# Performance work log

Measured on AMD Instinct MI355X. Metric: run time of the kernel, lower is better.

The kernel has to match this reference:

```python
import jax, jax.numpy as jnp
import numpy as np

B, C, W, H = 4, 64, 64, 64
CH = 64  # ch == input_nc so residual is valid

def setup_inputs() -> dict:
    key = jax.random.key(0)
    ks = jax.random.split(key, 5)
    return {
        "x": jax.random.normal(ks[0], (B, C, W, H), jnp.float32),
        "y": jax.random.normal(ks[1], (B, C, W, H), jnp.float32),
        "Wf": jax.random.normal(ks[2], (CH // 2, C), jnp.float32) * 0.05,
        "bf": jnp.zeros((CH // 2,), jnp.float32),
        "Wg": jax.random.normal(ks[3], (CH // 2, C), jnp.float32) * 0.05,
        "bg": jnp.zeros((CH // 2,), jnp.float32),
        "Wh": jax.random.normal(ks[4], (CH, C), jnp.float32) * 0.05,
        "bh": jnp.zeros((CH,), jnp.float32),
        "gamma": jnp.full((1,), 0.5, jnp.float32),
    }

def reference(x, y, Wf, bf, Wg, bg, Wh, bh, gamma):
    b, c, w, h = x.shape
    n = w * h
    xf = x.reshape(b, c, n)   # [b, C, N]
    yf = y.reshape(b, c, n)
    # 1x1 convs == per-pixel linear maps over channels
    f = jnp.einsum('oc,bcn->bon', Wf, xf) + bf[None, :, None]   # [b, CH/2, N]
    g = jnp.einsum('oc,bcn->bon', Wg, yf) + bg[None, :, None]   # [b, CH/2, N]
    hv = jnp.einsum('oc,bcn->bon', Wh, yf) + bh[None, :, None]  # [b, CH,   N]
    # s = g^T @ f : [b, N, N]
    s = jnp.einsum('bcm,bcn->bmn', g, f)
    beta = jax.nn.softmax(s, axis=-1)
    # o = beta @ h^T : [b, N, CH]
    o = jnp.einsum('bmn,bcn->bmc', beta, hv)
    o = o.transpose(0, 2, 1).reshape(b, -1, w, h)  # [b, CH, w, h]
    return gamma[0] * o + x
```

## Files before the change

### kernel.cpp

```cpp
#include <hip/hip_runtime.h>
#include <hip/hip_bf16.h>

#define BB  4
#define CC  64
#define NN  4096
#define CF  32
#define CHN 64

typedef __attribute__((ext_vector_type(8)))  __bf16 bf16x8;
typedef __attribute__((ext_vector_type(4)))  __bf16 bf16x4;
typedef __attribute__((ext_vector_type(4)))  float  floatx4;
typedef __attribute__((ext_vector_type(16))) float  floatx16;
typedef __attribute__((ext_vector_type(2)))  unsigned int uintx2;
typedef __attribute__((ext_vector_type(4)))  unsigned int uintx4;

__device__ __forceinline__ float scrub(float v) {
    return fminf(fmaxf(v, -1e30f), 1e30f);
}

__device__ __forceinline__ unsigned cvt_pk_bf16(float lo, float hi) {
    unsigned r;
    asm("v_cvt_pk_bf16_f32 %0, %1, %2" : "=v"(r) : "v"(lo), "v"(hi));
    return r;
}

__global__ __launch_bounds__(256) void prep_kernel(
    const float* __restrict__ x, const float* __restrict__ y,
    const float* __restrict__ Wf, const float* __restrict__ bfp,
    const float* __restrict__ Wg, const float* __restrict__ bgp,
    const float* __restrict__ Wh, const float* __restrict__ bhp,
    __bf16* __restrict__ fT, __bf16* __restrict__ gT, __bf16* __restrict__ hvb)
{
    __shared__ __align__(16) __bf16 wbf[128][72];
    __shared__ float sbias[128];

    const int t  = threadIdx.x;
    const int w  = t >> 6;
    const int l  = t & 63;
    const int lo = l & 15;
    const int q  = l >> 4;

    const int b   = blockIdx.x >> 7;
    const int nb  = blockIdx.x & 127;
    const int nn  = nb * 32 + (w & 1) * 16 + lo;
    const int ctbase = (w < 2) ? 0 : 4;

    for (int i = t; i < 128 * CC; i += 256) {
        int row = i >> 6, c = i & 63;
        float wv;
        if (row < 32)      wv = Wf[(size_t)row * CC + c];
        else if (row < 64) wv = Wg[(size_t)(row - 32) * CC + c];
        else               wv = Wh[(size_t)(row - 64) * CC + c];
        wbf[row][c] = (__bf16)wv;
    }
    if (t < 128) {
        if (t < 32)      sbias[t] = bfp[t];
        else if (t < 64) sbias[t] = bgp[t - 32];
        else             sbias[t] = bhp[t - 64];
    }
    __syncthreads();

    const float* xb = x + (size_t)b * CC * NN;
    const float* yb = y + (size_t)b * CC * NN;
    bf16x8 bx[2], by[2];
    #pragma unroll
    for (int kh = 0; kh < 2; kh++) {
        #pragma unroll
        for (int j = 0; j < 8; j++) {
            int c = kh * 32 + q * 8 + j;
            by[kh][j] = (__bf16)yb[(size_t)c * NN + nn];
        }
    }
    if (w < 2) {
        #pragma unroll
        for (int kh = 0; kh < 2; kh++)
            #pragma unroll
            for (int j = 0; j < 8; j++) {
                int c = kh * 32 + q * 8 + j;
                bx[kh][j] = (__bf16)xb[(size_t)c * NN + nn];
            }
    }

    const floatx4 zero4 = {0.f, 0.f, 0.f, 0.f};
    #pragma unroll
    for (int cti = 0; cti < 4; cti++) {
        const int ct = ctbase + cti;
        const bf16x8* src = (ct < 2) ? bx : by;
        floatx4 acc = zero4;
        #pragma unroll
        for (int kh = 0; kh < 2; kh++) {
            const bf16x8 a = *(const bf16x8*)&wbf[ct*16 + lo][kh*32 + q*8];
            acc = __builtin_amdgcn_mfma_f32_16x16x32_bf16(a, src[kh], acc, 0, 0, 0);
        }
        if (ct < 4) {
            bf16x4 pk;
            #pragma unroll
            for (int r = 0; r < 4; r++)
                pk[r] = (__bf16)(acc[r] + sbias[ct*16 + q*4 + r]);
            __bf16* dstbase = (ct < 2) ? fT : gT;
            int cho = (ct & 1) * 16;
            *(bf16x4*)&dstbase[((size_t)b * NN + nn) * CF + cho + q*4] = pk;
        } else {
            #pragma unroll
            for (int r = 0; r < 4; r++) {
                int ch = (ct - 4) * 16 + q*4 + r;
                hvb[((size_t)b * CHN + ch) * NN + nn] =
                    (__bf16)(acc[r] + sbias[64 + ch]);
            }
        }
    }
}

__global__ __launch_bounds__(512, 2) void attn_kernel(
    const __bf16* __restrict__ fT, const __bf16* __restrict__ gT,
    const __bf16* __restrict__ hvb,
    const float* __restrict__ x, const float* __restrict__ gamma_p,
    float* __restrict__ out)
{
    __shared__ float osum[8][64][67];
    __shared__ float lsum[512];

    const int t   = threadIdx.x;
    const int w   = t >> 6;
    const int l   = t & 63;
    const int l31 = l & 31;
    const int hi  = l >> 5;

    const int slot = blockIdx.x;
    const int xcd  = slot & 7;
    const int b    = xcd >> 1;
    const int mg   = ((xcd & 1) << 5) | (slot >> 3);
    const int m0   = mg * 64;

    const __bf16* fb = fT  + (size_t)b * NN * CF;
    const __bf16* gb = gT  + (size_t)b * NN * CF;
    const __bf16* hb = hvb + (size_t)b * CHN * NN;

    bf16x8 bg_[2][2];
    #pragma unroll
    for (int mt = 0; mt < 2; mt++)
        #pragma unroll
        for (int kk = 0; kk < 2; kk++)
            bg_[mt][kk] = *(const bf16x8*)(gb + (size_t)(m0 + mt*32 + l31) * CF + kk*16 + hi*8);

    const floatx16 zero16 = {};
    floatx16 oacc[2][2];
    #pragma unroll
    for (int mt = 0; mt < 2; mt++)
        #pragma unroll
        for (int ct = 0; ct < 2; ct++) oacc[mt][ct] = zero16;
    float rsum[2] = {0.f, 0.f};

    for (int i = 0; i < 8; i++) {
        const int n0 = (8*i + w) * 64;

        bf16x8 af[2][2];
        #pragma unroll
        for (int nt = 0; nt < 2; nt++)
            #pragma unroll
            for (int kk = 0; kk < 2; kk++)
                af[nt][kk] = *(const bf16x8*)(fb + (size_t)(n0 + nt*32 + l31) * CF + kk*16 + hi*8);

        bf16x8 bv[2][4];
        #pragma unroll
        for (int ct = 0; ct < 2; ct++)
            #pragma unroll
            for (int ks = 0; ks < 4; ks++)
                bv[ct][ks] = *(const bf16x8*)(hb + (size_t)(ct*32 + l31) * NN + n0 + ks*16 + hi*8);

        bf16x8 pa[2][4];
        #pragma unroll
        for (int mt = 0; mt < 2; mt++) {
            #pragma unroll
            for (int nt = 0; nt < 2; nt++) {
                floatx16 s = __builtin_amdgcn_mfma_f32_32x32x16_bf16(
                    af[nt][0], bg_[mt][0], zero16, 0, 0, 0);
                s = __builtin_amdgcn_mfma_f32_32x32x16_bf16(
                    af[nt][1], bg_[mt][1], s, 0, 0, 0);

                float p[16];
                #pragma unroll
                for (int r = 0; r < 16; r++) p[r] = __expf(s[r]);

                unsigned W[8];
                #pragma unroll
                for (int g = 0; g < 8; g++) W[g] = cvt_pk_bf16(p[2*g], p[2*g+1]);

                #pragma unroll
                for (int g = 0; g < 8; g++)
                    rsum[mt] += __uint_as_float(W[g] << 16)
                              + __uint_as_float(W[g] & 0xffff0000u);

                uintx2 s02 = __builtin_amdgcn_permlane32_swap(W[0], W[2], false, false);
                uintx2 s13 = __builtin_amdgcn_permlane32_swap(W[1], W[3], false, false);
                uintx2 s46 = __builtin_amdgcn_permlane32_swap(W[4], W[6], false, false);
                uintx2 s57 = __builtin_amdgcn_permlane32_swap(W[5], W[7], false, false);

                uintx4 w0 = {s02.x, s13.x, s02.y, s13.y};
                uintx4 w1 = {s46.x, s57.x, s46.y, s57.y};
                pa[mt][nt*2 + 0] = __builtin_bit_cast(bf16x8, w0);
                pa[mt][nt*2 + 1] = __builtin_bit_cast(bf16x8, w1);
            }
        }

        #pragma unroll
        for (int mt = 0; mt < 2; mt++)
            #pragma unroll
            for (int ct = 0; ct < 2; ct++)
                #pragma unroll
                for (int ks = 0; ks < 4; ks++)
                    oacc[mt][ct] = __builtin_amdgcn_mfma_f32_32x32x16_bf16(
                        pa[mt][ks], bv[ct][ks], oacc[mt][ct], 0, 0, 0);
    }

    #pragma unroll
    for (int mt = 0; mt < 2; mt++)
        rsum[mt] += __shfl_xor(rsum[mt], 32, 64);

    #pragma unroll
    for (int mt = 0; mt < 2; mt++) {
        #pragma unroll
        for (int ct = 0; ct < 2; ct++)
            #pragma unroll
            for (int r = 0; r < 16; r++)
                osum[w][mt*32 + ((r&3) + 8*(r>>2) + 4*hi)][ct*32 + l31] =
                    oacc[mt][ct][r];
        if (hi == 0)
            lsum[w*64 + mt*32 + l31] = rsum[mt];
    }
    __syncthreads();

    const float gam = gamma_p[0];
    const int m  = t & 63;
    const int cb = t >> 6;
    float lt = 0.f;
    #pragma unroll
    for (int s = 0; s < 8; s++) lt += lsum[s*64 + m];
    const float inv = 1.f / lt;
    #pragma unroll
    for (int it = 0; it < 8; it++) {
        const int ch = it*8 + cb;
        float acc = 0.f;
        #pragma unroll
        for (int s = 0; s < 8; s++) acc += osum[s][m][ch];
        size_t gi = ((size_t)b * CHN + ch) * NN + m0 + m;
        float ov = scrub(acc * inv);
        out[gi] = gam * ov + x[gi];
    }
}

extern "C" void kernel_launch(void* const* d_in, const int* in_sizes, int n_in,
                              void* d_out, int out_size, void* d_ws, size_t ws_size,
                              hipStream_t stream)
{
    const float* x     = (const float*)d_in[0];
    const float* y     = (const float*)d_in[1];
    const float* Wf    = (const float*)d_in[2];
    const float* bf    = (const float*)d_in[3];
    const float* Wg    = (const float*)d_in[4];
    const float* bg    = (const float*)d_in[5];
    const float* Wh    = (const float*)d_in[6];
    const float* bh    = (const float*)d_in[7];
    const float* gamma = (const float*)d_in[8];
    float* out = (float*)d_out;

    __bf16* wsb = (__bf16*)d_ws;
    __bf16* fT  = wsb;
    __bf16* gT  = fT + (size_t)BB * NN * CF;
    __bf16* hvb = gT + (size_t)BB * NN * CF;

    prep_kernel<<<dim3(BB * 128), dim3(256), 0, stream>>>(
        x, y, Wf, bf, Wg, bg, Wh, bh, fT, gT, hvb);
    attn_kernel<<<dim3(BB * 64), dim3(512), 0, stream>>>(
        fT, gT, hvb, x, gamma, out);
}
```

Baseline: 100.5 us.

## Fuse projection and attention kernels with a software grid barrier

Merges the prep and attention kernels into one persistent kernel of 256 blocks. A global atomic-counter grid barrier separates the 1x1-conv projection phase from the attention phase, and shared memory is reused between the two phases. Folds log2(e) into g so the softmax can use the raw v_exp_f32 instruction. The row sum now accumulates the fp32 exponentials instead of the bf16-rounded ones. This removes a kernel launch and the gap between kernels. The risk is a deadlock if all 256 blocks are not co-resident, plus the cost of barrier spinning.

```diff
diff --git a/kernel.cpp b/kernel.cpp
--- a/kernel.cpp
+++ b/kernel.cpp
@@ -6,6 +6,8 @@
 #define NN  4096
 #define CF  32
 #define CHN 64
+
+#define LOG2E 1.4426950408889634f
 
 typedef __attribute__((ext_vector_type(8)))  __bf16 bf16x8;
 typedef __attribute__((ext_vector_type(4)))  __bf16 bf16x4;
@@ -23,114 +25,136 @@
     asm("v_cvt_pk_bf16_f32 %0, %1, %2" : "=v"(r) : "v"(lo), "v"(hi));
     return r;
 }
-
-__global__ __launch_bounds__(256) void prep_kernel(
+__device__ __forceinline__ float exp2_f32(float x) {
+    float r;
+    asm("v_exp_f32 %0, %1" : "=v"(r) : "v"(x));
+    return r;
+}
+
+__device__ unsigned g_cnt = 0;
+__device__ unsigned g_gen = 0;
+
+__device__ __forceinline__ void grid_barrier() {
+    __syncthreads();
+    if (threadIdx.x == 0) {
+        __threadfence();
+        unsigned my = atomicAdd(&g_cnt, 1u);
+        unsigned target = (my >> 8) + 1;
+        if ((my & 255u) == 255u) {
+            __hip_atomic_store(&g_gen, target, __ATOMIC_RELEASE,
+                               __HIP_MEMORY_SCOPE_AGENT);
+        } else {
+            while ((int)(__hip_atomic_load(&g_gen, __ATOMIC_ACQUIRE,
+                                           __HIP_MEMORY_SCOPE_AGENT) - target) < 0)
+                __builtin_amdgcn_s_sleep(1);
+        }
+        __threadfence();
+    }
+    __syncthreads();
+}
+
+__global__ __launch_bounds__(512, 2) void fused_kernel(
     const float* __restrict__ x, const float* __restrict__ y,
     const float* __restrict__ Wf, const float* __restrict__ bfp,
     const float* __restrict__ Wg, const float* __restrict__ bgp,
     const float* __restrict__ Wh, const float* __restrict__ bhp,
-    __bf16* __restrict__ fT, __bf16* __restrict__ gT, __bf16* __restrict__ hvb)
+    __bf16* __restrict__ fT, __bf16* __restrict__ gT, __bf16* __restrict__ hvb,
+    const float* __restrict__ gamma_p, float* __restrict__ out)
 {
-    __shared__ __align__(16) __bf16 wbf[128][72];
-    __shared__ float sbias[128];
-
-    const int t  = threadIdx.x;
-    const int w  = t >> 6;
-    const int l  = t & 63;
-    const int lo = l & 15;
-    const int q  = l >> 4;
-
-    const int b   = blockIdx.x >> 7;
-    const int nb  = blockIdx.x & 127;
-    const int nn  = nb * 32 + (w & 1) * 16 + lo;
-    const int ctbase = (w < 2) ? 0 : 4;
-
-    for (int i = t; i < 128 * CC; i += 256) {
-        int row = i >> 6, c = i & 63;
-        float wv;
-        if (row < 32)      wv = Wf[(size_t)row * CC + c];
-        else if (row < 64) wv = Wg[(size_t)(row - 32) * CC + c];
-        else               wv = Wh[(size_t)(row - 64) * CC + c];
-        wbf[row][c] = (__bf16)wv;
-    }
-    if (t < 128) {
-        if (t < 32)      sbias[t] = bfp[t];
-        else if (t < 64) sbias[t] = bgp[t - 32];
-        else             sbias[t] = bhp[t - 64];
-    }
-    __syncthreads();
-
-    const float* xb = x + (size_t)b * CC * NN;
-    const float* yb = y + (size_t)b * CC * NN;
-    bf16x8 bx[2], by[2];
-    #pragma unroll
-    for (int kh = 0; kh < 2; kh++) {
-        #pragma unroll
-        for (int j = 0; j < 8; j++) {
-            int c = kh * 32 + q * 8 + j;
-            by[kh][j] = (__bf16)yb[(size_t)c * NN + nn];
-        }
-    }
-    if (w < 2) {
+    __shared__ __align__(16) char smem[8*64*67*4 + 512*4];
+    __bf16 (*wbf)[72]      = (__bf16 (*)[72])smem;
+    float*  sbias          = (float*)(smem + 128*72*2);
+    float (*osum)[64][67]  = (float (*)[64][67])smem;
+    float*  lsum           = (float*)(smem + 8*64*67*4);
+
+    const int t = threadIdx.x;
+
+    const int slot = blockIdx.x;
+    const int xcd  = slot & 7;
+    const int b    = xcd >> 1;
+    const int mg   = ((xcd & 1) << 5) | (slot >> 3);
+
+    {
+        const int w  = t >> 6;
+        const int l  = t & 63;
+        const int lo = l & 15;
+        const int q  = l >> 4;
+        const int nn = mg * 64 + (w & 3) * 16 + lo;
+        const int ctbase = (w >> 2) * 4;
+
+        for (int i = t; i < 128 * CC; i += 512) {
+            int row = i >> 6, c = i & 63;
+            float wv;
+            if (row < 32)      wv = Wf[(size_t)row * CC + c];
+            else if (row < 64) wv = Wg[(size_t)(row - 32) * CC + c];
+            else               wv = Wh[(size_t)(row - 64) * CC + c];
+            wbf[row][c] = (__bf16)wv;
+        }
+        if (t < 128) {
+            if (t < 32)      sbias[t] = bfp[t];
+            else if (t < 64) sbias[t] = bgp[t - 32];
+            else             sbias[t] = bhp[t - 64];
+        }
+        __syncthreads();
+
+        const float* xb = x + (size_t)b * CC * NN;
+        const float* yb = y + (size_t)b * CC * NN;
+        bf16x8 bx[2], by[2];
         #pragma unroll
         for (int kh = 0; kh < 2; kh++)
             #pragma unroll
             for (int j = 0; j < 8; j++) {
                 int c = kh * 32 + q * 8 + j;
-                bx[kh][j] = (__bf16)xb[(size_t)c * NN + nn];
-            }
-    }
-
-    const floatx4 zero4 = {0.f, 0.f, 0.f, 0.f};
-    #pragma unroll
-    for (int cti = 0; cti < 4; cti++) {
-        const int ct = ctbase + cti;
-        const bf16x8* src = (ct < 2) ? bx : by;
-        floatx4 acc = zero4;
-        #pragma unroll
-        for (int kh = 0; kh < 2; kh++) {
-            const bf16x8 a = *(const bf16x8*)&wbf[ct*16 + lo][kh*32 + q*8];
-            acc = __builtin_amdgcn_mfma_f32_16x16x32_bf16(a, src[kh], acc, 0, 0, 0);
-        }
-        if (ct < 4) {
-            bf16x4 pk;
-            #pragma unroll
-            for (int r = 0; r < 4; r++)
-                pk[r] = (__bf16)(acc[r] + sbias[ct*16 + q*4 + r]);
-            __bf16* dstbase = (ct < 2) ? fT : gT;
-            int cho = (ct & 1) * 16;
-            *(bf16x4*)&dstbase[((size_t)b * NN + nn) * CF + cho + q*4] = pk;
-        } else {
-            #pragma unroll
-            for (int r = 0; r < 4; r++) {
-                int ch = (ct - 4) * 16 + q*4 + r;
-                hvb[((size_t)b * CHN + ch) * NN + nn] =
-                    (__bf16)(acc[r] + sbias[64 + ch]);
-            }
-        }
-    }
-}
-
-__global__ __launch_bounds__(512, 2) void attn_kernel(
-    const __bf16* __restrict__ fT, const __bf16* __restrict__ gT,
-    const __bf16* __restrict__ hvb,
-    const float* __restrict__ x, const float* __restrict__ gamma_p,
-    float* __restrict__ out)
-{
-    __shared__ float osum[8][64][67];
-    __shared__ float lsum[512];
-
-    const int t   = threadIdx.x;
+                by[kh][j] = (__bf16)yb[(size_t)c * NN + nn];
+            }
+        if (ctbase == 0) {
+            #pragma unroll
+            for (int kh = 0; kh < 2; kh++)
+                #pragma unroll
+                for (int j = 0; j < 8; j++) {
+                    int c = kh * 32 + q * 8 + j;
+                    bx[kh][j] = (__bf16)xb[(size_t)c * NN + nn];
+                }
+        }
+
+        const floatx4 zero4 = {0.f, 0.f, 0.f, 0.f};
+        #pragma unroll
+        for (int cti = 0; cti < 4; cti++) {
+            const int ct = ctbase + cti;
+            const bf16x8* src = (ct < 2) ? bx : by;
+            floatx4 acc = zero4;
+            #pragma unroll
+            for (int kh = 0; kh < 2; kh++) {
+                const bf16x8 a = *(const bf16x8*)&wbf[ct*16 + lo][kh*32 + q*8];
+                acc = __builtin_amdgcn_mfma_f32_16x16x32_bf16(a, src[kh], acc, 0, 0, 0);
+            }
+            if (ct < 4) {
+                const float sc = (ct < 2) ? 1.0f : LOG2E;
+                bf16x4 pk;
+                #pragma unroll
+                for (int r = 0; r < 4; r++)
+                    pk[r] = (__bf16)((acc[r] + sbias[ct*16 + q*4 + r]) * sc);
+                __bf16* dstbase = (ct < 2) ? fT : gT;
+                int cho = (ct & 1) * 16;
+                *(bf16x4*)&dstbase[((size_t)b * NN + nn) * CF + cho + q*4] = pk;
+            } else {
+                #pragma unroll
+                for (int r = 0; r < 4; r++) {
+                    int ch = (ct - 4) * 16 + q*4 + r;
+                    hvb[((size_t)b * CHN + ch) * NN + nn] =
+                        (__bf16)(acc[r] + sbias[64 + ch]);
+                }
+            }
+        }
+    }
+
+    grid_barrier();
+
     const int w   = t >> 6;
     const int l   = t & 63;
     const int l31 = l & 31;
     const int hi  = l >> 5;
-
-    const int slot = blockIdx.x;
-    const int xcd  = slot & 7;
-    const int b    = xcd >> 1;
-    const int mg   = ((xcd & 1) << 5) | (slot >> 3);
-    const int m0   = mg * 64;
+    const int m0  = mg * 64;
 
     const __bf16* fb = fT  + (size_t)b * NN * CF;
     const __bf16* gb = gT  + (size_t)b * NN * CF;
@@ -180,16 +204,14 @@
 
                 float p[16];
                 #pragma unroll
-                for (int r = 0; r < 16; r++) p[r] = __expf(s[r]);
+                for (int r = 0; r < 16; r++) p[r] = exp2_f32(s[r]);
+
+                #pragma unroll
+                for (int r = 0; r < 16; r++) rsum[mt] += p[r];
 
                 unsigned W[8];
                 #pragma unroll
                 for (int g = 0; g < 8; g++) W[g] = cvt_pk_bf16(p[2*g], p[2*g+1]);
-
-                #pragma unroll
-                for (int g = 0; g < 8; g++)
-                    rsum[mt] += __uint_as_float(W[g] << 16)
-                              + __uint_as_float(W[g] & 0xffff0000u);
 
                 uintx2 s02 = __builtin_amdgcn_permlane32_swap(W[0], W[2], false, false);
                 uintx2 s13 = __builtin_amdgcn_permlane32_swap(W[1], W[3], false, false);
@@ -217,6 +239,7 @@
     for (int mt = 0; mt < 2; mt++)
         rsum[mt] += __shfl_xor(rsum[mt], 32, 64);
 
+    __syncthreads();
     #pragma unroll
     for (int mt = 0; mt < 2; mt++) {
         #pragma unroll
@@ -269,8 +292,6 @@
     __bf16* gT  = fT + (size_t)BB * NN * CF;
     __bf16* hvb = gT + (size_t)BB * NN * CF;
 
-    prep_kernel<<<dim3(BB * 128), dim3(256), 0, stream>>>(
-        x, y, Wf, bf, Wg, bg, Wh, bh, fT, gT, hvb);
-    attn_kernel<<<dim3(BB * 64), dim3(512), 0, stream>>>(
-        fT, gT, hvb, x, gamma, out);
-}
+    fused_kernel<<<dim3(256), dim3(512), 0, stream>>>(
+        x, y, Wf, bf, Wg, bg, Wh, bh, fT, gT, hvb, gamma, out);
+}
```

Result: slower. 122.1 us (+21.5%).

## Tile fT/gT/hv layouts for coalesced loads and fold log2e into g

Applied to the files above, without the earlier changes.

The prep kernel now writes f, g and hv in a blocked layout that matches the MFMA operand fragments. Each lane's 16-byte load in the attention kernel becomes contiguous with its neighbours, replacing row-strided gathers. g is pre-scaled by log2(e) so the softmax uses the raw v_exp_f32 exp2 instruction instead of __expf. The row sum now accumulates the fp32 exponentials instead of the bf16-rounded values, which slightly changes how the normalisation matches the weights fed to the MFMA.

```diff
diff --git a/kernel.cpp b/kernel.cpp
--- a/kernel.cpp
+++ b/kernel.cpp
@@ -6,6 +6,8 @@
 #define NN  4096
 #define CF  32
 #define CHN 64
+
+#define LOG2E 1.4426950408889634f
 
 typedef __attribute__((ext_vector_type(8)))  __bf16 bf16x8;
 typedef __attribute__((ext_vector_type(4)))  __bf16 bf16x4;
@@ -23,6 +25,12 @@
     asm("v_cvt_pk_bf16_f32 %0, %1, %2" : "=v"(r) : "v"(lo), "v"(hi));
     return r;
 }
+__device__ __forceinline__ float exp2_f32(float x) {
+    float r;
+    asm("v_exp_f32 %0, %1" : "=v"(r) : "v"(x));
+    return r;
+}
+
 
 __global__ __launch_bounds__(256) void prep_kernel(
     const float* __restrict__ x, const float* __restrict__ y,
@@ -64,14 +72,13 @@
     const float* yb = y + (size_t)b * CC * NN;
     bf16x8 bx[2], by[2];
     #pragma unroll
-    for (int kh = 0; kh < 2; kh++) {
+    for (int kh = 0; kh < 2; kh++)
         #pragma unroll
         for (int j = 0; j < 8; j++) {
             int c = kh * 32 + q * 8 + j;
             by[kh][j] = (__bf16)yb[(size_t)c * NN + nn];
         }
-    }
-    if (w < 2) {
+    if (ctbase == 0) {
         #pragma unroll
         for (int kh = 0; kh < 2; kh++)
             #pragma unroll
@@ -93,18 +100,24 @@
             acc = __builtin_amdgcn_mfma_f32_16x16x32_bf16(a, src[kh], acc, 0, 0, 0);
         }
         if (ct < 4) {
+            const float sc = (ct < 2) ? 1.0f : LOG2E;
             bf16x4 pk;
             #pragma unroll
             for (int r = 0; r < 4; r++)
-                pk[r] = (__bf16)(acc[r] + sbias[ct*16 + q*4 + r]);
+                pk[r] = (__bf16)((acc[r] + sbias[ct*16 + q*4 + r]) * sc);
             __bf16* dstbase = (ct < 2) ? fT : gT;
-            int cho = (ct & 1) * 16;
-            *(bf16x4*)&dstbase[((size_t)b * NN + nn) * CF + cho + q*4] = pk;
+            const int c0 = (ct & 1) * 16 + q * 4;
+            const int off = (nn >> 5)*1024 + (c0 >> 4)*512 + (nn & 31)*16
+                          + ((c0 >> 3) & 1)*8 + (c0 & 7);
+            *(bf16x4*)&dstbase[(size_t)b * NN * CF + off] = pk;
         } else {
             #pragma unroll
             for (int r = 0; r < 4; r++) {
                 int ch = (ct - 4) * 16 + q*4 + r;
-                hvb[((size_t)b * CHN + ch) * NN + nn] =
+                const int off = (nn >> 6)*4096 + (ch >> 5)*2048
+                              + ((nn >> 4) & 3)*512 + (ch & 31)*16
+                              + ((nn >> 3) & 1)*8 + (nn & 7);
+                hvb[(size_t)b * CHN * NN + off] =
                     (__bf16)(acc[r] + sbias[64 + ch]);
             }
         }
@@ -136,12 +149,14 @@
     const __bf16* gb = gT  + (size_t)b * NN * CF;
     const __bf16* hb = hvb + (size_t)b * CHN * NN;
 
+    const int lane16 = (l31 * 2 + hi) * 8;
+
     bf16x8 bg_[2][2];
     #pragma unroll
     for (int mt = 0; mt < 2; mt++)
         #pragma unroll
         for (int kk = 0; kk < 2; kk++)
-            bg_[mt][kk] = *(const bf16x8*)(gb + (size_t)(m0 + mt*32 + l31) * CF + kk*16 + hi*8);
+            bg_[mt][kk] = *(const bf16x8*)(gb + (size_t)(mg*2 + mt)*1024 + kk*512 + lane16);
 
     const floatx16 zero16 = {};
     floatx16 oacc[2][2];
@@ -152,21 +167,21 @@
     float rsum[2] = {0.f, 0.f};
 
     for (int i = 0; i < 8; i++) {
-        const int n0 = (8*i + w) * 64;
+        const int nc = 8*i + w;
 
         bf16x8 af[2][2];
         #pragma unroll
         for (int nt = 0; nt < 2; nt++)
             #pragma unroll
             for (int kk = 0; kk < 2; kk++)
-                af[nt][kk] = *(const bf16x8*)(fb + (size_t)(n0 + nt*32 + l31) * CF + kk*16 + hi*8);
+                af[nt][kk] = *(const bf16x8*)(fb + (size_t)(nc*2 + nt)*1024 + kk*512 + lane16);
 
         bf16x8 bv[2][4];
         #pragma unroll
         for (int ct = 0; ct < 2; ct++)
             #pragma unroll
             for (int ks = 0; ks < 4; ks++)
-                bv[ct][ks] = *(const bf16x8*)(hb + (size_t)(ct*32 + l31) * NN + n0 + ks*16 + hi*8);
+                bv[ct][ks] = *(const bf16x8*)(hb + (size_t)nc*4096 + ct*2048 + ks*512 + lane16);
 
         bf16x8 pa[2][4];
         #pragma unroll
@@ -180,16 +195,14 @@
 
                 float p[16];
                 #pragma unroll
-                for (int r = 0; r < 16; r++) p[r] = __expf(s[r]);
+                for (int r = 0; r < 16; r++) p[r] = exp2_f32(s[r]);
+
+                #pragma unroll
+                for (int r = 0; r < 16; r++) rsum[mt] += p[r];
 
                 unsigned W[8];
                 #pragma unroll
                 for (int g = 0; g < 8; g++) W[g] = cvt_pk_bf16(p[2*g], p[2*g+1]);
-
-                #pragma unroll
-                for (int g = 0; g < 8; g++)
-                    rsum[mt] += __uint_as_float(W[g] << 16)
-                              + __uint_as_float(W[g] & 0xffff0000u);
 
                 uintx2 s02 = __builtin_amdgcn_permlane32_swap(W[0], W[2], false, false);
                 uintx2 s13 = __builtin_amdgcn_permlane32_swap(W[1], W[3], false, false);
```

New measurement: 92.79 us (median of 3 runs). -7.7%, faster.
